# Kernel optimization log

Measured on AMD Instinct MI355X. Metric: run time of the kernel, lower is better.

## Reference

```python
import jax, jax.numpy as jnp
import numpy as np

T = 0.07  # temperature from init default


def _l2norm(x):
    return x / jnp.linalg.norm(x, axis=1, keepdims=True)


def setup_inputs() -> dict:
    key = jax.random.key(0)
    ks = jax.random.split(key, 12)
    B, D, K = 512, 128, 4096
    G = M = 131072
    return {
        "feat": jax.random.normal(ks[0], (B, D), jnp.float32),
        "label": jax.random.randint(ks[1], (B,), 0, 2),
        "out": jnp.zeros((B, K + 1), jnp.float32),   # unused by forward
        "name": jnp.arange(B),                        # unused by forward
        "y": jax.random.randint(ks[2], (B,), 0, G),   # unused by forward
        "memory_feat_gbm": jax.random.normal(ks[3], (G, D), jnp.float32),
        "memory_prob_gbm": jax.random.uniform(ks[4], (G,), jnp.float32),
        "memory_feat_mate": jax.random.normal(ks[5], (M, D), jnp.float32),
        "memory_prob_mate": jax.random.uniform(ks[6], (M,), jnp.float32),
        "idx_n_g": jax.random.randint(ks[7], (K, 1), 0, G),
        "idx_p_g": jax.random.randint(ks[8], (1, 1), 0, G // 4),
        "idx_n_m": jax.random.randint(ks[9], (K, 1), 0, M),
        "idx_p_m": jax.random.randint(ks[10], (1, 1), 0, M // 4),
    }


def reference(feat, label, out, name, y, memory_feat_gbm, memory_prob_gbm,
              memory_feat_mate, memory_prob_mate, idx_n_g, idx_p_g, idx_n_m, idx_p_m):
    # __init__ normalizes the memory banks once
    mfg = _l2norm(memory_feat_gbm)
    mfm = _l2norm(memory_feat_mate)
    feat_n = _l2norm(feat)  # [B, D]
    output_size = mfg.shape[0]

    # gather positive / negative prototypes (all rows unit-norm, so
    # cosine_similarity == dot product)
    wp_g = mfg[idx_p_g.ravel()]   # [1, D]
    wn_g = mfg[idx_n_g.ravel()]   # [K, D]
    wp_m = mfm[idx_p_m.ravel()]   # [1, D]
    wn_m = mfm[idx_n_m.ravel()]   # [K, D]

    # label==0 (gbm): pos from gbm bank, negs from mate bank; label==1 mirrored
    row_gbm = jnp.concatenate([feat_n @ wp_g.T, feat_n @ wn_m.T], axis=1)   # [B, K+1]
    row_mate = jnp.concatenate([feat_n @ wp_m.T, feat_n @ wn_g.T], axis=1)  # [B, K+1]
    sims = jnp.where((label == 0)[:, None], row_gbm, row_mate)

    # use_softmax=False path: exp(s/T) / Z with Z set from first batch (treated as constant)
    e = jnp.exp(sims / T)
    Z = jax.lax.stop_gradient(e.mean() * output_size)
    out_feature_p_n = e / Z

    # confident cluster members + current batch (data-dependent sizes; eager jax)
    mask_g = memory_prob_gbm > 0.5
    mask_m = memory_prob_mate > 0.6
    feature_clu_all = jnp.concatenate([mfg[mask_g], mfm[mask_m], feat_n], axis=0)
    gt_clu_all = jnp.concatenate([
        jnp.zeros((int(mask_g.sum()),), label.dtype),
        jnp.ones((int(mask_m.sum()),), label.dtype),
        label,
    ], axis=0)
    return out_feature_p_n, feature_clu_all, gt_clu_all
```

## Files before the change

### kernel.cpp

```cpp
#include <hip/hip_runtime.h>
#include <math.h>


#define TINV 14.2857142857142857f
#define JT 64
#define BT 32

__device__ __forceinline__ float wredsum64(float v) {
#pragma unroll
  for (int m = 32; m > 0; m >>= 1) v += __shfl_xor(v, m, 64);
  return v;
}

__global__ __launch_bounds__(256) void k_stageA(
    const float* __restrict__ feat, const int* __restrict__ label,
    const float* __restrict__ mfg, const float* __restrict__ pg,
    const float* __restrict__ mfm, const float* __restrict__ pm,
    const int* __restrict__ idxpg, const int* __restrict__ idxpm,
    float* __restrict__ outp, long long cluTail, long long gtTail,
    int* __restrict__ bucket, int* __restrict__ n0p,
    int* __restrict__ cg, int* __restrict__ cm,
    float* __restrict__ posPartials,
    int B, int K1, int G, int M,
    int nCountBlk, int nFeatBlk, int nPosBlk) {
  int bid = blockIdx.x, t = threadIdx.x;

  if (bid < nCountBlk) {
    __shared__ int s[8];
    int i = bid * 256 + t;
    int a = (i < G) && (pg[i] > 0.5f);
    int b = (i < M) && (pm[i] > 0.6f);
    unsigned long long ba = __ballot(a), bb = __ballot(b);
    int lane = t & 63, w = t >> 6;
    if (lane == 0) { s[w] = __popcll(ba); s[4 + w] = __popcll(bb); }
    __syncthreads();
    if (t == 0) cg[bid] = s[0] + s[1] + s[2] + s[3];
    if (t == 1) cm[bid] = s[4] + s[5] + s[6] + s[7];
    return;
  }
  bid -= nCountBlk;

  if (bid < nFeatBlk) {
    int gid = bid * 256 + t;
    int w = gid >> 6, lane = gid & 63;
    if (w < B) {
      float2 v = ((const float2*)feat)[(long long)w * 64 + lane];
      float sq = wredsum64(v.x * v.x + v.y * v.y);
      float inv = rsqrtf(sq);
      ((float2*)(outp + cluTail))[(long long)w * 64 + lane] =
          make_float2(v.x * inv, v.y * inv);
      if (lane == 0) outp[gtTail + w] = (float)label[w];
    }
    return;
  }
  bid -= nFeatBlk;

  if (bid < nPosBlk) {
    __shared__ float ps[4];
    int gid = bid * 256 + t;
    int w = gid >> 6, lane = gid & 63, lw = t >> 6;
    float e = 0.f;
    if (w < B) {
      int lab = label[w];
      const float* bank = lab ? mfm : mfg;
      long long row = lab ? idxpm[0] : idxpg[0];
      float2 wv = ((const float2*)(bank + row * 128))[lane];
      float2 fv = ((const float2*)feat)[(long long)w * 64 + lane];
      float dot = wredsum64(fv.x * wv.x + fv.y * wv.y);
      float sqw = wredsum64(wv.x * wv.x + wv.y * wv.y);
      float sqf = wredsum64(fv.x * fv.x + fv.y * fv.y);
      e = expf(dot * rsqrtf(sqw) * rsqrtf(sqf) * TINV);
      if (lane == 0) outp[(long long)w * K1] = e;
    }
    if (lane == 0) ps[lw] = e;
    __syncthreads();
    if (t == 0) posPartials[bid] = ps[0] + ps[1] + ps[2] + ps[3];
    return;
  }

  {
    __shared__ int sc[512];
    int t2 = t + 256;
    int m0 = (t < B) ? (label[t] == 0 ? 1 : 0) : 0;
    int m1 = (t2 < B) ? (label[t2] == 0 ? 1 : 0) : 0;
    sc[t] = m0; sc[t2] = m1;
    __syncthreads();
    for (int off = 1; off < 512; off <<= 1) {
      int u0 = (t >= off) ? sc[t - off] : 0;
      int u1 = (t2 >= off) ? sc[t2 - off] : 0;
      __syncthreads();
      sc[t] += u0; sc[t2] += u1;
      __syncthreads();
    }
    int n0 = (B > 0) ? sc[B - 1] : 0;
    if (t < B) {
      int incl = sc[t];
      if (m0) bucket[incl - 1] = t; else bucket[n0 + t - incl] = t;
    }
    if (t2 < B) {
      int incl = sc[t2];
      if (m1) bucket[incl - 1] = t2; else bucket[n0 + t2 - incl] = t2;
    }
    if (t == 0) *n0p = n0;
  }
}

__global__ __launch_bounds__(256) void k_stageB(
    const float* __restrict__ featn, const int* __restrict__ bucket,
    const int* __restrict__ n0ptr,
    const float* __restrict__ mfg, const float* __restrict__ mfm,
    const int* __restrict__ idxng, const int* __restrict__ idxnm,
    float* __restrict__ out0, float* __restrict__ partials,
    int B, int K, int K1, int simsGx) {
  __shared__ float4 wl[JT][33];
  __shared__ float4 fl[BT][33];
  __shared__ float invw[JT];
  __shared__ float bs[4];
  int t = threadIdx.x;
  int pidx = (int)blockIdx.x;
  int bx = pidx % simsGx, by = pidx / simsGx;
  int n0 = *n0ptr;
  int nb0 = (n0 + BT - 1) / BT;
  int lab, p0, cnt;
  if (by < nb0) {
    lab = 0; p0 = by * BT; cnt = min(BT, n0 - p0);
  } else {
    int k = by - nb0; p0 = n0 + k * BT;
    int n1 = B - n0; cnt = min(BT, n1 - k * BT); lab = 1;
  }
  if (cnt <= 0) { if (t == 0) partials[pidx] = 0.f; return; }
  const float* bank = lab == 0 ? mfm : mfg;
  const int* idxN   = lab == 0 ? idxnm : idxng;
  int j0 = bx * JT;

#pragma unroll
  for (int q = 0; q < 8; q++) {
    int lin = q * 256 + t;
    int row = lin >> 5, col = lin & 31;
    long long srow = idxN[j0 + row];
    wl[row][col] = ((const float4*)(bank + srow * 128))[col];
  }
#pragma unroll
  for (int q = 0; q < 4; q++) {
    int lin = q * 256 + t;
    int row = lin >> 5, col = lin & 31;
    float4 v = make_float4(0.f, 0.f, 0.f, 0.f);
    if (row < cnt) {
      int bg = bucket[p0 + row];
      v = ((const float4*)(featn + (long long)bg * 128))[col];
    }
    fl[row][col] = v;
  }
  __syncthreads();

  {
    int r = t >> 2, q = t & 3;
    float ss = 0.f;
#pragma unroll
    for (int c = 0; c < 8; c++) {
      float4 v = wl[r][q * 8 + c];
      ss += v.x * v.x + v.y * v.y + v.z * v.z + v.w * v.w;
    }
    ss += __shfl_xor(ss, 1, 64);
    ss += __shfl_xor(ss, 2, 64);
    if (q == 0) invw[r] = rsqrtf(ss);
  }
  __syncthreads();

  int tj = t & 15, tb = t >> 4;
  float acc[4][2];
#pragma unroll
  for (int a = 0; a < 4; a++)
#pragma unroll
    for (int b = 0; b < 2; b++) acc[a][b] = 0.f;

#pragma unroll 4
  for (int i = 0; i < 32; i++) {
    float4 w0 = wl[tj][i];
    float4 w1 = wl[tj + 16][i];
    float4 w2 = wl[tj + 32][i];
    float4 w3 = wl[tj + 48][i];
    float4 f0 = fl[tb][i];
    float4 f1 = fl[tb + 16][i];
    acc[0][0] += w0.x*f0.x + w0.y*f0.y + w0.z*f0.z + w0.w*f0.w;
    acc[1][0] += w1.x*f0.x + w1.y*f0.y + w1.z*f0.z + w1.w*f0.w;
    acc[2][0] += w2.x*f0.x + w2.y*f0.y + w2.z*f0.z + w2.w*f0.w;
    acc[3][0] += w3.x*f0.x + w3.y*f0.y + w3.z*f0.z + w3.w*f0.w;
    acc[0][1] += w0.x*f1.x + w0.y*f1.y + w0.z*f1.z + w0.w*f1.w;
    acc[1][1] += w1.x*f1.x + w1.y*f1.y + w1.z*f1.z + w1.w*f1.w;
    acc[2][1] += w2.x*f1.x + w2.y*f1.y + w2.z*f1.z + w2.w*f1.w;
    acc[3][1] += w3.x*f1.x + w3.y*f1.y + w3.z*f1.z + w3.w*f1.w;
  }

  float mysum = 0.f;
#pragma unroll
  for (int bb = 0; bb < 2; bb++) {
    int bl = tb + 16 * bb;
    if (bl < cnt) {
      int bg = bucket[p0 + bl];
#pragma unroll
      for (int jj = 0; jj < 4; jj++) {
        int jr = tj + 16 * jj;
        float e = expf(acc[jj][bb] * invw[jr] * TINV);
        out0[(long long)bg * K1 + 1 + j0 + jr] = e;
        mysum += e;
      }
    }
  }
  float wsum = wredsum64(mysum);
  if ((t & 63) == 0) bs[t >> 6] = wsum;
  __syncthreads();
  if (t == 0) partials[pidx] = bs[0] + bs[1] + bs[2] + bs[3];
}

__global__ __launch_bounds__(256) void k_stageD(
    const float* __restrict__ mfg, const float* __restrict__ mfm,
    const float* __restrict__ pg, const float* __restrict__ pm,
    const int* __restrict__ cg, const int* __restrict__ cm,
    float* __restrict__ outp, long long cluBase, long long gtBase,
    int G, int M, int NB, int nGatherBlk,
    float* __restrict__ out0, const float* __restrict__ partials, int nPart,
    double factor, long long n4) {
  int t = threadIdx.x;

  if ((int)blockIdx.x < nGatherBlk) {
    __shared__ int red[4];
    __shared__ int woff[4];
    __shared__ int selRow[256];
    int bid = blockIdx.x;
    int bankId = bid / NB;
    int cb = bid - bankId * NB;
    const float* probs = bankId ? pm : pg;
    const float* rows  = bankId ? mfm : mfg;
    float thr = bankId ? 0.6f : 0.5f;
    int Nelem = bankId ? M : G;
    int lane = t & 63, w = t >> 6;

    int j0 = t, j1 = t + 256;
    int s = 0;
    if (bankId == 0) {
      if (j0 < cb) s += cg[j0];
      if (j1 < cb && j1 < NB) s += cg[j1];
    } else {
      if (j0 < NB) s += cg[j0];
      if (j1 < NB) s += cg[j1];
      if (j0 < cb) s += cm[j0];
      if (j1 < cb && j1 < NB) s += cm[j1];
    }
#pragma unroll
    for (int m = 32; m > 0; m >>= 1) s += __shfl_xor(s, m, 64);
    if (lane == 0) red[w] = s;

    int i = cb * 256 + t;
    int f = (i < Nelem) && (probs[i] > thr);
    unsigned long long mb = __ballot(f);
    if (lane == 0) woff[w] = __popcll(mb);
    __syncthreads();

    long long off = (long long)red[0] + red[1] + red[2] + red[3];
    int pre = 0;
#pragma unroll
    for (int q = 0; q < 3; q++)
      if (q < w) pre += woff[q];
    int S = woff[0] + woff[1] + woff[2] + woff[3];
    unsigned long long below = lane ? ((~0ull) >> (64 - lane)) : 0ull;
    if (f) selRow[pre + __popcll(mb & below)] = i;
    __syncthreads();
    if (S == 0) return;

    float labv = (float)bankId;
    int hw = t >> 5, l = t & 31;
    for (int r0 = hw * 4; r0 < S; r0 += 32) {
      int r1 = r0 + 1, r2 = r0 + 2, r3 = r0 + 3;
      int s0 = selRow[r0];
      int s1 = selRow[r1 < S ? r1 : r0];
      int s2 = selRow[r2 < S ? r2 : r0];
      int s3 = selRow[r3 < S ? r3 : r0];
      float4 v0 = ((const float4*)(rows + (long long)s0 * 128))[l];
      float4 v1 = ((const float4*)(rows + (long long)s1 * 128))[l];
      float4 v2 = ((const float4*)(rows + (long long)s2 * 128))[l];
      float4 v3 = ((const float4*)(rows + (long long)s3 * 128))[l];
      float q0 = v0.x*v0.x + v0.y*v0.y + v0.z*v0.z + v0.w*v0.w;
      float q1 = v1.x*v1.x + v1.y*v1.y + v1.z*v1.z + v1.w*v1.w;
      float q2 = v2.x*v2.x + v2.y*v2.y + v2.z*v2.z + v2.w*v2.w;
      float q3 = v3.x*v3.x + v3.y*v3.y + v3.z*v3.z + v3.w*v3.w;
#pragma unroll
      for (int m = 16; m > 0; m >>= 1) {
        q0 += __shfl_xor(q0, m, 64);
        q1 += __shfl_xor(q1, m, 64);
        q2 += __shfl_xor(q2, m, 64);
        q3 += __shfl_xor(q3, m, 64);
      }
      float i0 = rsqrtf(q0), i1 = rsqrtf(q1), i2 = rsqrtf(q2), i3 = rsqrtf(q3);
      long long d0 = off + r0;
      ((float4*)(outp + cluBase + d0 * 128))[l] =
          make_float4(v0.x*i0, v0.y*i0, v0.z*i0, v0.w*i0);
      if (l == 0) outp[gtBase + d0] = labv;
      if (r1 < S) {
        long long d = off + r1;
        ((float4*)(outp + cluBase + d * 128))[l] =
            make_float4(v1.x*i1, v1.y*i1, v1.z*i1, v1.w*i1);
        if (l == 0) outp[gtBase + d] = labv;
      }
      if (r2 < S) {
        long long d = off + r2;
        ((float4*)(outp + cluBase + d * 128))[l] =
            make_float4(v2.x*i2, v2.y*i2, v2.z*i2, v2.w*i2);
        if (l == 0) outp[gtBase + d] = labv;
      }
      if (r3 < S) {
        long long d = off + r3;
        ((float4*)(outp + cluBase + d * 128))[l] =
            make_float4(v3.x*i3, v3.y*i3, v3.z*i3, v3.w*i3);
        if (l == 0) outp[gtBase + d] = labv;
      }
    }
    return;
  }

  __shared__ double sd[256];
  double s = 0.0;
  for (int i = t; i < nPart; i += 256) s += (double)partials[i];
  sd[t] = s;
  __syncthreads();
  for (int off = 128; off > 0; off >>= 1) {
    if (t < off) sd[t] += sd[t + off];
    __syncthreads();
  }
  float sc = (float)(factor / sd[0]);
  long long base = (long long)((int)blockIdx.x - nGatherBlk) * 256 + t;
  long long stride = (long long)(gridDim.x - nGatherBlk) * 256;
  for (long long i = base; i < n4; i += stride) {
    float4 v = ((float4*)out0)[i];
    v.x *= sc; v.y *= sc; v.z *= sc; v.w *= sc;
    ((float4*)out0)[i] = v;
  }
}

extern "C" void kernel_launch(void* const* d_in, const int* in_sizes, int n_in,
                              void* d_out, int out_size, void* d_ws,
                              size_t ws_size, hipStream_t stream) {
  const float* feat  = (const float*)d_in[0];
  const int*   label = (const int*)d_in[1];
  const float* mfg   = (const float*)d_in[5];
  const float* pg    = (const float*)d_in[6];
  const float* mfm   = (const float*)d_in[7];
  const float* pm    = (const float*)d_in[8];
  const int*   idxng = (const int*)d_in[9];
  const int*   idxpg = (const int*)d_in[10];
  const int*   idxnm = (const int*)d_in[11];
  const int*   idxpm = (const int*)d_in[12];
  float* outp = (float*)d_out;

  const int B = in_sizes[1];
  const int D = 128;
  const int K = in_sizes[9];
  const int G = in_sizes[6];
  const int M = in_sizes[8];
  const int K1 = K + 1;

  const long long C0 = (long long)B * K1;
  const long long R = ((long long)out_size - C0) / (D + 1);
  const long long G0 = C0 + R * D;
  const long long cluTail = C0 + (R - B) * (long long)D;
  const long long gtTail = G0 + (R - B);

  const float* featn = outp + cluTail;

  char* wsb = (char*)d_ws;
  size_t o = 0;
  auto alloc = [&](size_t bytes) -> char* {
    char* p = wsb + o;
    o = (o + bytes + 255) & ~(size_t)255;
    return p;
  };
  const int simsGx = K / JT;
  const int simsGy = B / BT + 1;
  const int nPartSims = simsGx * simsGy;
  const int nPosBlk = (B * 64 + 255) / 256;
  float* partials = (float*)alloc(sizeof(float) * (nPartSims + nPosBlk));
  int* bucket = (int*)alloc(sizeof(int) * B);
  int* n0p = (int*)alloc(sizeof(int) * 4);
  const int NB = ((G > M ? G : M) + 255) / 256;
  int* cg = (int*)alloc(sizeof(int) * NB);
  int* cm = (int*)alloc(sizeof(int) * NB);
  (void)ws_size; (void)n_in;

  const int nFeatBlk = (B * 64 + 255) / 256;
  const int gridA = NB + nFeatBlk + nPosBlk + 1;
  const int gridB = nPartSims;
  const int nGatherBlk = 2 * NB;
  const int nScaleBlk = 1024;
  const int gridD = nGatherBlk + nScaleBlk;

  k_stageA<<<gridA, 256, 0, stream>>>(
      feat, label, mfg, pg, mfm, pm, idxpg, idxpm,
      outp, cluTail, gtTail, bucket, n0p, cg, cm,
      partials + nPartSims, B, K1, G, M, NB, nFeatBlk, nPosBlk);

  k_stageB<<<gridB, 256, 0, stream>>>(
      featn, bucket, n0p, mfg, mfm, idxng, idxnm,
      outp, partials, B, K, K1, simsGx);

  double factor = (double)B * (double)K1 / (double)G;
  k_stageD<<<gridD, 256, 0, stream>>>(
      mfg, mfm, pg, pm, cg, cm, outp, C0, G0, G, M, NB, nGatherBlk,
      outp, partials, nPartSims + nPosBlk, factor, C0 / 4);
}
```

Baseline: 53.67 us.

## Compute negative similarities with bf16 MFMA and a larger batch tile

Replaces the scalar fp32 FMA dot-product loop in the similarity stage with bf16 MFMA 16x16x32 instructions on XOR-swizzled LDS tiles. Gathered rows are converted to bf16 as they are loaded, and the row-norm reduction is folded into that load, which removes one barrier. The batch tile grows from 32 to 64 rows, so the grid shrinks. Dot products now use bf16 inputs, which loses precision before the exp(s/0.07), and that amplifies errors and may exceed tolerance.

```diff
diff --git a/kernel.cpp b/kernel.cpp
--- a/kernel.cpp
+++ b/kernel.cpp
@@ -4,12 +4,30 @@
 
 #define TINV 14.2857142857142857f
 #define JT 64
-#define BT 32
+#define BT2 64
+
+typedef __attribute__((ext_vector_type(8))) short bfrag;
+typedef __attribute__((ext_vector_type(4))) float ffrag;
 
 __device__ __forceinline__ float wredsum64(float v) {
 #pragma unroll
   for (int m = 32; m > 0; m >>= 1) v += __shfl_xor(v, m, 64);
   return v;
+}
+
+__device__ __forceinline__ unsigned short f2bf(float x) {
+  unsigned u = __float_as_uint(x);
+  u += 0x7fffu + ((u >> 16) & 1u);
+  return (unsigned short)(u >> 16);
+}
+
+__device__ __forceinline__ bfrag ldsread(const short* base, int row, int kb) {
+  return *(const bfrag*)((const char*)base + row * 256 +
+                         (kb ^ ((row & 7) << 4)));
+}
+__device__ __forceinline__ void ldswrite(short* base, int row, int kb,
+                                         bfrag v) {
+  *(bfrag*)((char*)base + row * 256 + (kb ^ ((row & 7) << 4))) = v;
 }
 
 __global__ __launch_bounds__(256) void k_stageA(
@@ -112,21 +130,21 @@
     const int* __restrict__ idxng, const int* __restrict__ idxnm,
     float* __restrict__ out0, float* __restrict__ partials,
     int B, int K, int K1, int simsGx) {
-  __shared__ float4 wl[JT][33];
-  __shared__ float4 fl[BT][33];
-  __shared__ float invw[JT];
+  __shared__ __align__(16) short wlds[64 * 128];
+  __shared__ __align__(16) short flds[64 * 128];
+  __shared__ float invw[64];
   __shared__ float bs[4];
   int t = threadIdx.x;
   int pidx = (int)blockIdx.x;
   int bx = pidx % simsGx, by = pidx / simsGx;
   int n0 = *n0ptr;
-  int nb0 = (n0 + BT - 1) / BT;
+  int nb0 = (n0 + BT2 - 1) / BT2;
   int lab, p0, cnt;
   if (by < nb0) {
-    lab = 0; p0 = by * BT; cnt = min(BT, n0 - p0);
+    lab = 0; p0 = by * BT2; cnt = min(BT2, n0 - p0);
   } else {
-    int k = by - nb0; p0 = n0 + k * BT;
-    int n1 = B - n0; cnt = min(BT, n1 - k * BT); lab = 1;
+    int k = by - nb0; p0 = n0 + k * BT2;
+    int n1 = B - n0; cnt = min(BT2, n1 - k * BT2); lab = 1;
   }
   if (cnt <= 0) { if (t == 0) partials[pidx] = 0.f; return; }
   const float* bank = lab == 0 ? mfm : mfg;
@@ -134,79 +152,85 @@
   int j0 = bx * JT;
 
 #pragma unroll
-  for (int q = 0; q < 8; q++) {
-    int lin = q * 256 + t;
-    int row = lin >> 5, col = lin & 31;
+  for (int q = 0; q < 4; q++) {
+    int slot = q * 256 + t;
+    int row = slot >> 4, ch = slot & 15;
     long long srow = idxN[j0 + row];
-    wl[row][col] = ((const float4*)(bank + srow * 128))[col];
+    const float4* gp = (const float4*)(bank + srow * 128 + ch * 8);
+    float4 x0 = gp[0], x1 = gp[1];
+    bfrag h;
+    h[0] = (short)f2bf(x0.x); h[1] = (short)f2bf(x0.y);
+    h[2] = (short)f2bf(x0.z); h[3] = (short)f2bf(x0.w);
+    h[4] = (short)f2bf(x1.x); h[5] = (short)f2bf(x1.y);
+    h[6] = (short)f2bf(x1.z); h[7] = (short)f2bf(x1.w);
+    ldswrite(wlds, row, ch * 16, h);
+    float s = x0.x*x0.x + x0.y*x0.y + x0.z*x0.z + x0.w*x0.w +
+              x1.x*x1.x + x1.y*x1.y + x1.z*x1.z + x1.w*x1.w;
+    s += __shfl_xor(s, 1, 64);
+    s += __shfl_xor(s, 2, 64);
+    s += __shfl_xor(s, 4, 64);
+    s += __shfl_xor(s, 8, 64);
+    if (ch == 0) invw[row] = rsqrtf(s);
   }
 #pragma unroll
   for (int q = 0; q < 4; q++) {
-    int lin = q * 256 + t;
-    int row = lin >> 5, col = lin & 31;
-    float4 v = make_float4(0.f, 0.f, 0.f, 0.f);
+    int slot = q * 256 + t;
+    int row = slot >> 4, ch = slot & 15;
+    bfrag h;
+#pragma unroll
+    for (int i = 0; i < 8; i++) h[i] = 0;
     if (row < cnt) {
       int bg = bucket[p0 + row];
-      v = ((const float4*)(featn + (long long)bg * 128))[col];
-    }
-    fl[row][col] = v;
+      const float4* gp = (const float4*)(featn + (long long)bg * 128 + ch * 8);
+      float4 x0 = gp[0], x1 = gp[1];
+      h[0] = (short)f2bf(x0.x); h[1] = (short)f2bf(x0.y);
+      h[2] = (short)f2bf(x0.z); h[3] = (short)f2bf(x0.w);
+      h[4] = (short)f2bf(x1.x); h[5] = (short)f2bf(x1.y);
+      h[6] = (short)f2bf(x1.z); h[7] = (short)f2bf(x1.w);
+    }
+    ldswrite(flds, row, ch * 16, h);
   }
   __syncthreads();
 
-  {
-    int r = t >> 2, q = t & 3;
-    float ss = 0.f;
-#pragma unroll
-    for (int c = 0; c < 8; c++) {
-      float4 v = wl[r][q * 8 + c];
-      ss += v.x * v.x + v.y * v.y + v.z * v.z + v.w * v.w;
-    }
-    ss += __shfl_xor(ss, 1, 64);
-    ss += __shfl_xor(ss, 2, 64);
-    if (q == 0) invw[r] = rsqrtf(ss);
-  }
-  __syncthreads();
-
-  int tj = t & 15, tb = t >> 4;
-  float acc[4][2];
-#pragma unroll
-  for (int a = 0; a < 4; a++)
-#pragma unroll
-    for (int b = 0; b < 2; b++) acc[a][b] = 0.f;
-
-#pragma unroll 4
-  for (int i = 0; i < 32; i++) {
-    float4 w0 = wl[tj][i];
-    float4 w1 = wl[tj + 16][i];
-    float4 w2 = wl[tj + 32][i];
-    float4 w3 = wl[tj + 48][i];
-    float4 f0 = fl[tb][i];
-    float4 f1 = fl[tb + 16][i];
-    acc[0][0] += w0.x*f0.x + w0.y*f0.y + w0.z*f0.z + w0.w*f0.w;
-    acc[1][0] += w1.x*f0.x + w1.y*f0.y + w1.z*f0.z + w1.w*f0.w;
-    acc[2][0] += w2.x*f0.x + w2.y*f0.y + w2.z*f0.z + w2.w*f0.w;
-    acc[3][0] += w3.x*f0.x + w3.y*f0.y + w3.z*f0.z + w3.w*f0.w;
-    acc[0][1] += w0.x*f1.x + w0.y*f1.y + w0.z*f1.z + w0.w*f1.w;
-    acc[1][1] += w1.x*f1.x + w1.y*f1.y + w1.z*f1.z + w1.w*f1.w;
-    acc[2][1] += w2.x*f1.x + w2.y*f1.y + w2.z*f1.z + w2.w*f1.w;
-    acc[3][1] += w3.x*f1.x + w3.y*f1.y + w3.z*f1.z + w3.w*f1.w;
+  int l = t & 63, wv = t >> 6;
+  int wj = wv & 1, wb = wv >> 1;
+  int colb = l & 15, kg = l >> 4;
+  ffrag acc00 = {0.f, 0.f, 0.f, 0.f};
+  ffrag acc01 = {0.f, 0.f, 0.f, 0.f};
+  ffrag acc10 = {0.f, 0.f, 0.f, 0.f};
+  ffrag acc11 = {0.f, 0.f, 0.f, 0.f};
+#pragma unroll
+  for (int ks = 0; ks < 4; ks++) {
+    int kb = ks * 64 + kg * 16;
+    bfrag a0 = ldsread(flds, wb * 32 + colb,      kb);
+    bfrag a1 = ldsread(flds, wb * 32 + 16 + colb, kb);
+    bfrag b0 = ldsread(wlds, wj * 32 + colb,      kb);
+    bfrag b1 = ldsread(wlds, wj * 32 + 16 + colb, kb);
+    acc00 = __builtin_amdgcn_mfma_f32_16x16x32_bf16(a0, b0, acc00, 0, 0, 0);
+    acc01 = __builtin_amdgcn_mfma_f32_16x16x32_bf16(a0, b1, acc01, 0, 0, 0);
+    acc10 = __builtin_amdgcn_mfma_f32_16x16x32_bf16(a1, b0, acc10, 0, 0, 0);
+    acc11 = __builtin_amdgcn_mfma_f32_16x16x32_bf16(a1, b1, acc11, 0, 0, 0);
   }
 
   float mysum = 0.f;
-#pragma unroll
-  for (int bb = 0; bb < 2; bb++) {
-    int bl = tb + 16 * bb;
-    if (bl < cnt) {
-      int bg = bucket[p0 + bl];
-#pragma unroll
-      for (int jj = 0; jj < 4; jj++) {
-        int jr = tj + 16 * jj;
-        float e = expf(acc[jj][bb] * invw[jr] * TINV);
-        out0[(long long)bg * K1 + 1 + j0 + jr] = e;
+  int rowg = l >> 4;
+  auto epi = [&](const ffrag& A, int bt, int jt) {
+    int bl = wb * 32 + bt * 16 + rowg * 4;
+    int jl = wj * 32 + jt * 16 + colb;
+    float iw = invw[jl];
+#pragma unroll
+    for (int r = 0; r < 4; r++) {
+      int b2 = bl + r;
+      if (b2 < cnt) {
+        int bg = bucket[p0 + b2];
+        float e = expf(A[r] * iw * TINV);
+        out0[(long long)bg * K1 + 1 + j0 + jl] = e;
         mysum += e;
       }
     }
-  }
+  };
+  epi(acc00, 0, 0); epi(acc01, 0, 1); epi(acc10, 1, 0); epi(acc11, 1, 1);
+
   float wsum = wredsum64(mysum);
   if ((t & 63) == 0) bs[t >> 6] = wsum;
   __syncthreads();
@@ -375,7 +399,7 @@
     return p;
   };
   const int simsGx = K / JT;
-  const int simsGy = B / BT + 1;
+  const int simsGy = B / BT2 + 2;
   const int nPartSims = simsGx * simsGy;
   const int nPosBlk = (B * 64 + 255) / 256;
   float* partials = (float*)alloc(sizeof(float) * (nPartSims + nPosBlk));
```

Measured after the change: 44.76 us, median of 2. 16.6% less time.
